# Performance work log

Hardware: AMD Instinct MI355X
Metric: run time of the kernel (lower is better)

Reference implementation:

```python
import jax, jax.numpy as jnp
import numpy as np

B, L, D, H, A = 4, 2048, 1024, 16, 64  # batch, seq, d_model, n_head, d_head


def setup_inputs() -> dict:
    key = jax.random.key(0)
    ks = jax.random.split(key, 6)
    scale = 1.0 / np.sqrt(D)
    return {
        "xq": jax.random.normal(ks[0], (B, L, D), dtype=jnp.float32),
        "xkv": jax.random.normal(ks[1], (B, L, D), dtype=jnp.float32),
        "Q": jax.random.normal(ks[2], (D, H, A), dtype=jnp.float32) * scale,
        "K": jax.random.normal(ks[3], (D, H, A), dtype=jnp.float32) * scale,
        "V": jax.random.normal(ks[4], (D, H, A), dtype=jnp.float32) * scale,
        "O": jax.random.normal(ks[5], (D, H, A), dtype=jnp.float32) * scale,
    }


def reference(xq, xkv, Q, K, V, O):
    # embed: 'dha, ...ld -> ...lha'
    q = jnp.einsum('dha,bld->blha', Q, xq)
    k = jnp.einsum('dha,bld->blha', K, xkv)
    v = jnp.einsum('dha,bld->blha', V, xkv)
    # outer: '...lha, ...mha -> ...hlm'  (full LxL score matrix, no scaling in source)
    scores = jnp.einsum('blha,bmha->bhlm', q, k)
    attn = jax.nn.softmax(scores, axis=-1)  # dropout p=0 (eval)
    # score: '...hlm, ...mha -> ...lha'
    ctx = jnp.einsum('bhlm,bmha->blha', attn, v)
    # output: '...dha, ...lha -> ...ld'
    return jnp.einsum('dha,blha->bld', O, ctx)
```

## Files before the change

### kernel.cpp

```cpp
#include <hip/hip_runtime.h>
#include <math.h>

typedef __bf16 bf16;
typedef bf16 bf16x8 __attribute__((ext_vector_type(8)));
typedef bf16 bf16x4 __attribute__((ext_vector_type(4)));
typedef float f32x4 __attribute__((ext_vector_type(4)));
typedef float f32x16 __attribute__((ext_vector_type(16)));

#define B_ 4
#define L_ 2048
#define D_ 1024
#define H_ 16
#define A_ 64
#define HA_ 1024
#define BL_ 8192
#define LOG2E 1.44269504088896340736f

__device__ __forceinline__ void gload16(const void* g, void* l) {
  __builtin_amdgcn_global_load_lds((const __attribute__((address_space(1))) void*)g,
                                   (__attribute__((address_space(3))) void*)l,
                                   16, 0, 0);
}

__device__ __forceinline__ unsigned cvt_pk_bf16(float lo, float hi) {
  unsigned r;
  asm volatile("v_cvt_pk_bf16_f32 %0, %1, %2" : "=v"(r) : "v"(lo), "v"(hi));
  return r;
}

__device__ __forceinline__ void permswap(unsigned& a, unsigned& b) {
  asm volatile("v_permlane32_swap_b32 %0, %1" : "+v"(a), "+v"(b));
}

__global__ __launch_bounds__(256) void cast_all(const float* __restrict__ xq,
                                                const float* __restrict__ xkv,
                                                const float* __restrict__ ow,
                                                bf16* __restrict__ xq_b,
                                                bf16* __restrict__ xkv_b,
                                                bf16* __restrict__ wo_b) {
  const int NX = BL_ * D_ / 8;
  const int NW = D_ * HA_ / 8;
  int i = blockIdx.x * blockDim.x + threadIdx.x;
  const float* src;
  bf16* dst;
  int j;
  if (i < NX) { src = xq; dst = xq_b; j = i; }
  else if (i < 2 * NX) { src = xkv; dst = xkv_b; j = i - NX; }
  else if (i < 2 * NX + NW) { src = ow; dst = wo_b; j = i - 2 * NX; }
  else return;
  const float4* s = reinterpret_cast<const float4*>(src) + (size_t)j * 2;
  float4 a = s[0], b = s[1];
  bf16x8 o;
  o[0] = (bf16)a.x; o[1] = (bf16)a.y; o[2] = (bf16)a.z; o[3] = (bf16)a.w;
  o[4] = (bf16)b.x; o[5] = (bf16)b.y; o[6] = (bf16)b.z; o[7] = (bf16)b.w;
  *reinterpret_cast<bf16x8*>(dst + (size_t)j * 8) = o;
}

__global__ __launch_bounds__(256) void transpose_cast_w3(const float* __restrict__ wq,
                                                         const float* __restrict__ wk,
                                                         const float* __restrict__ wv,
                                                         bf16* __restrict__ oq,
                                                         bf16* __restrict__ ok,
                                                         bf16* __restrict__ ov) {
  __shared__ float tile[32][33];
  const int z = blockIdx.z;
  const float* w = (z == 0) ? wq : (z == 1) ? wk : wv;
  bf16* wt = (z == 0) ? oq : (z == 1) ? ok : ov;
  const float scale = (z == 0) ? LOG2E : 1.0f;
  const int d0 = blockIdx.y * 32, h0 = blockIdx.x * 32;
  const int tx = threadIdx.x, ty = threadIdx.y;
  #pragma unroll
  for (int j = 0; j < 4; j++)
    tile[ty + j * 8][tx] = w[(size_t)(d0 + ty + j * 8) * HA_ + h0 + tx];
  __syncthreads();
  #pragma unroll
  for (int j = 0; j < 4; j++)
    wt[(size_t)(h0 + ty + j * 8) * D_ + d0 + tx] = (bf16)(tile[tx][ty + j * 8] * scale);
}

template <int MODE>
__device__ __forceinline__ void gemm_bt_core(const bf16* __restrict__ Ap,
                                             const bf16* __restrict__ Bp,
                                             void* __restrict__ Cp,
                                             int m0, int n0) {
  const int K = 1024;
  __shared__ __align__(16) bf16 As[128 * 32];
  __shared__ __align__(16) bf16 Bs[128 * 32];
  const int tid = threadIdx.x;
  const int lane = tid & 63, w = tid >> 6;
  const int wr = w >> 1, wc = w & 1;
  const int g = lane >> 4, c = lane & 15;
  f32x4 acc[4][4] = {};
  const int srow = tid >> 2, sch = tid & 3;
  const int sw0 = (sch ^ (srow & 3)) * 8;
  for (int k0 = 0; k0 < K; k0 += 32) {
    gload16(Ap + (size_t)(m0 + srow) * K + k0 + sw0, As + tid * 8);
    gload16(Ap + (size_t)(m0 + 64 + srow) * K + k0 + sw0, As + (256 + tid) * 8);
    gload16(Bp + (size_t)(n0 + srow) * K + k0 + sw0, Bs + tid * 8);
    gload16(Bp + (size_t)(n0 + 64 + srow) * K + k0 + sw0, Bs + (256 + tid) * 8);
    __syncthreads();
    bf16x8 af[4], bfr[4];
    #pragma unroll
    for (int m = 0; m < 4; m++)
      af[m] = *reinterpret_cast<const bf16x8*>(As + (wr * 64 + m * 16 + c) * 32 + ((g ^ (c & 3)) * 8));
    #pragma unroll
    for (int n = 0; n < 4; n++)
      bfr[n] = *reinterpret_cast<const bf16x8*>(Bs + (wc * 64 + n * 16 + c) * 32 + ((g ^ (c & 3)) * 8));
    #pragma unroll
    for (int m = 0; m < 4; m++)
      #pragma unroll
      for (int n = 0; n < 4; n++)
        acc[m][n] = __builtin_amdgcn_mfma_f32_16x16x32_bf16(af[m], bfr[n], acc[m][n], 0, 0, 0);
    __syncthreads();
  }
  #pragma unroll
  for (int m = 0; m < 4; m++) {
    #pragma unroll
    for (int n = 0; n < 4; n++) {
      if (MODE == 2) {
        int row0 = m0 + wr * 64 + m * 16 + g * 4;
        int col = n0 + wc * 64 + n * 16 + c;
        int b = row0 >> 11, l0 = row0 & 2047, h = col >> 6, a = col & 63;
        bf16x4 o4;
        #pragma unroll
        for (int i = 0; i < 4; i++) o4[i] = (bf16)acc[m][n][i];
        *reinterpret_cast<bf16x4*>((bf16*)Cp + ((size_t)(b * H_ + h) * A_ + a) * L_ + l0) = o4;
      } else {
        #pragma unroll
        for (int i = 0; i < 4; i++) {
          int row = m0 + wr * 64 + m * 16 + g * 4 + i;
          int col = n0 + wc * 64 + n * 16 + c;
          float v = acc[m][n][i];
          if (MODE == 0) {
            int b = row >> 11, l = row & 2047, h = col >> 6, a = col & 63;
            ((bf16*)Cp)[(((size_t)b * H_ + h) * L_ + l) * A_ + a] = (bf16)v;
          } else {
            ((float*)Cp)[(size_t)row * 1024 + col] = v;
          }
        }
      }
    }
  }
}

__device__ __forceinline__ void xcd_mn(int id, int& m0, int& n0) {
  int xcd = id & 7, j = id >> 3;
  m0 = (xcd * 8 + (j >> 3)) * 128;
  n0 = (j & 7) * 128;
}

__global__ __launch_bounds__(256, 2) void gemm_proj(const bf16* xq_b, const bf16* xkv_b,
                                                    const bf16* wq, const bf16* wk, const bf16* wv,
                                                    bf16* qb, bf16* kb, bf16* vtb) {
  int m0, n0;
  xcd_mn(blockIdx.x, m0, n0);
  const int z = blockIdx.z;
  if (z == 0)      gemm_bt_core<0>(xq_b, wq, qb, m0, n0);
  else if (z == 1) gemm_bt_core<0>(xkv_b, wk, kb, m0, n0);
  else             gemm_bt_core<2>(xkv_b, wv, vtb, m0, n0);
}

__global__ __launch_bounds__(256, 2) void gemm_out_k(const bf16* ctx, const bf16* wo, float* out) {
  int m0, n0;
  xcd_mn(blockIdx.x, m0, n0);
  gemm_bt_core<1>(ctx, wo, out, m0, n0);
}

__device__ __forceinline__ void pa_build(const f32x16& s, bf16x8& f0, bf16x8& f1) {
  #pragma unroll
  for (int sl = 0; sl < 2; sl++) {
    unsigned a0 = cvt_pk_bf16(s[8 * sl + 0], s[8 * sl + 1]);
    unsigned b0 = cvt_pk_bf16(s[8 * sl + 4], s[8 * sl + 5]);
    permswap(a0, b0);
    unsigned a1 = cvt_pk_bf16(s[8 * sl + 2], s[8 * sl + 3]);
    unsigned b1 = cvt_pk_bf16(s[8 * sl + 6], s[8 * sl + 7]);
    permswap(a1, b1);
    uint4 v; v.x = a0; v.y = a1; v.z = b0; v.w = b1;
    if (sl == 0) f0 = __builtin_bit_cast(bf16x8, v);
    else         f1 = __builtin_bit_cast(bf16x8, v);
  }
}

__global__ __launch_bounds__(512, 2) void attn_kernel(const bf16* __restrict__ qg,
                                                      const bf16* __restrict__ kg,
                                                      const bf16* __restrict__ vtg,
                                                      bf16* __restrict__ ctx) {
  __shared__ __align__(16) bf16 Ks[2][64 * 64];
  __shared__ __align__(16) bf16 Vs[2][64 * 64];
  const int tid = threadIdx.x;
  const int lane = tid & 63;
  const int w = tid >> 6;
  const int c = lane & 31;
  const int hi = lane >> 5;
  const int cs7 = c & 7;
  const int bh = blockIdx.x;
  const int q0 = blockIdx.y * 256;
  const bf16* qh = qg + (size_t)bh * L_ * A_;
  const bf16* kh = kg + (size_t)bh * L_ * A_;
  const bf16* vh = vtg + (size_t)bh * A_ * L_;

  const int qrow = q0 + w * 32 + c;
  bf16x8 qf[4];
  #pragma unroll
  for (int ds = 0; ds < 4; ds++)
    qf[ds] = *reinterpret_cast<const bf16x8*>(qh + (size_t)qrow * A_ + ds * 16 + hi * 8);

  bf16x8 ones;
  #pragma unroll
  for (int j = 0; j < 8; j++) ones[j] = (bf16)1.0f;

  f32x16 oacc0 = {}, oacc1 = {};
  f32x16 ssum = {};

  int koA[4], koB[4];
  #pragma unroll
  for (int ds = 0; ds < 4; ds++) {
    koA[ds] = c * 64 + ((2 * ds + hi) ^ cs7) * 8;
    koB[ds] = (32 + c) * 64 + ((2 * ds + hi) ^ cs7) * 8;
  }

  const int sr = tid >> 3, sc = tid & 7;
  const int ss = (sc ^ (sr & 7)) * 8;
  const bf16* ksrc = kh + (size_t)sr * A_ + ss;
  const bf16* vsrc = vh + (size_t)sr * L_ + ss;

  gload16(ksrc, &Ks[0][tid * 8]);
  gload16(vsrc, &Vs[0][tid * 8]);
  __syncthreads();
  int cur = 0;

  for (int t = 0; t < L_ / 64; t++) {
    if (t < L_ / 64 - 1) {
      gload16(ksrc + (size_t)(t + 1) * 4096, &Ks[cur ^ 1][tid * 8]);
      gload16(vsrc + (size_t)(t + 1) * 64, &Vs[cur ^ 1][tid * 8]);
    }
    const bf16* Kc = Ks[cur];
    const bf16* Vc = Vs[cur];

    f32x16 s0 = {}, s1 = {};
    __builtin_amdgcn_s_setprio(1);
    #pragma unroll
    for (int ds = 0; ds < 4; ds++) {
      bf16x8 k0 = *reinterpret_cast<const bf16x8*>(Kc + koA[ds]);
      bf16x8 k1 = *reinterpret_cast<const bf16x8*>(Kc + koB[ds]);
      s0 = __builtin_amdgcn_mfma_f32_32x32x16_bf16(k0, qf[ds], s0, 0, 0, 0);
      s1 = __builtin_amdgcn_mfma_f32_32x32x16_bf16(k1, qf[ds], s1, 0, 0, 0);
    }
    __builtin_amdgcn_s_setprio(0);

    #pragma unroll
    for (int r = 0; r < 16; r++) {
      s0[r] = __builtin_amdgcn_exp2f(s0[r]);
      s1[r] = __builtin_amdgcn_exp2f(s1[r]);
    }

    bf16x8 paf0, paf1, paf2, paf3;
    pa_build(s0, paf0, paf1);
    pa_build(s1, paf2, paf3);

    __builtin_amdgcn_s_setprio(1);
    #pragma unroll
    for (int ks = 0; ks < 4; ks++) {
      const bf16x8 pa = (ks == 0) ? paf0 : (ks == 1) ? paf1 : (ks == 2) ? paf2 : paf3;
      bf16x8 v0 = *reinterpret_cast<const bf16x8*>(Vc + koA[ks]);
      bf16x8 v1 = *reinterpret_cast<const bf16x8*>(Vc + koB[ks]);
      oacc0 = __builtin_amdgcn_mfma_f32_32x32x16_bf16(v0, pa, oacc0, 0, 0, 0);
      oacc1 = __builtin_amdgcn_mfma_f32_32x32x16_bf16(v1, pa, oacc1, 0, 0, 0);
      ssum = __builtin_amdgcn_mfma_f32_32x32x16_bf16(ones, pa, ssum, 0, 0, 0);
    }
    __builtin_amdgcn_s_setprio(0);

    __syncthreads();
    cur ^= 1;
  }

  float inv = 1.f / ssum[0];
  const int b = bh >> 4, h = bh & 15;
  bf16* crow = ctx + (((size_t)b * L_ + qrow) * H_ + h) * A_;
  #pragma unroll
  for (int n = 0; n < 2; n++) {
    #pragma unroll
    for (int rq = 0; rq < 4; rq++) {
      bf16x4 o4;
      #pragma unroll
      for (int j = 0; j < 4; j++) {
        float v = (n == 0) ? oacc0[rq * 4 + j] : oacc1[rq * 4 + j];
        o4[j] = (bf16)(v * inv);
      }
      *reinterpret_cast<bf16x4*>(crow + n * 32 + rq * 8 + hi * 4) = o4;
    }
  }
}

extern "C" void kernel_launch(void* const* d_in, const int* in_sizes, int n_in,
                              void* d_out, int out_size, void* d_ws, size_t ws_size,
                              hipStream_t stream) {
  const float* xq = (const float*)d_in[0];
  const float* xkv = (const float*)d_in[1];
  const float* Qw = (const float*)d_in[2];
  const float* Kw = (const float*)d_in[3];
  const float* Vw = (const float*)d_in[4];
  const float* Ow = (const float*)d_in[5];
  float* out = (float*)d_out;

  char* ws = (char*)d_ws;
  const size_t SZ16 = (size_t)BL_ * HA_ * sizeof(bf16);
  const size_t SZW = (size_t)D_ * HA_ * sizeof(bf16);
  bf16* xq_b = (bf16*)(ws);
  bf16* xkv_b = (bf16*)(ws + SZ16);
  bf16* wq_t = (bf16*)(ws + 2 * SZ16);
  bf16* wk_t = (bf16*)(ws + 2 * SZ16 + SZW);
  bf16* wv_t = (bf16*)(ws + 2 * SZ16 + 2 * SZW);
  bf16* wo_b = (bf16*)(ws + 2 * SZ16 + 3 * SZW);
  bf16* qb = (bf16*)(ws + 2 * SZ16 + 4 * SZW);
  bf16* kb = qb + (size_t)BL_ * HA_;
  bf16* vtb = kb + (size_t)BL_ * HA_;
  bf16* ctxb = xkv_b;

  const int NCAST = (2 * BL_ * D_ + D_ * HA_) / 8;
  cast_all<<<(NCAST + 255) / 256, 256, 0, stream>>>(xq, xkv, Ow, xq_b, xkv_b, wo_b);
  transpose_cast_w3<<<dim3(32, 32, 3), dim3(32, 8), 0, stream>>>(Qw, Kw, Vw, wq_t, wk_t, wv_t);

  gemm_proj<<<dim3(512, 1, 3), 256, 0, stream>>>(xq_b, xkv_b, wq_t, wk_t, wv_t, qb, kb, vtb);
  attn_kernel<<<dim3(64, 8), 512, 0, stream>>>(qb, kb, vtb, ctxb);
  gemm_out_k<<<512, 256, 0, stream>>>(ctxb, wo_b, out);
}
```

Measured before the change: 194.9 us.

## Merge cast and weight-transpose kernels; fuse K and V projections sharing A tile

```diff
diff --git a/kernel.cpp b/kernel.cpp
--- a/kernel.cpp
+++ b/kernel.cpp
@@ -15,6 +15,7 @@
 #define HA_ 1024
 #define BL_ 8192
 #define LOG2E 1.44269504088896340736f
+#define NCASTB 8704
 
 __device__ __forceinline__ void gload16(const void* g, void* l) {
   __builtin_amdgcn_global_load_lds((const __attribute__((address_space(1))) void*)g,
@@ -32,50 +33,54 @@
   asm volatile("v_permlane32_swap_b32 %0, %1" : "+v"(a), "+v"(b));
 }
 
-__global__ __launch_bounds__(256) void cast_all(const float* __restrict__ xq,
+__global__ __launch_bounds__(256) void prep_all(const float* __restrict__ xq,
                                                 const float* __restrict__ xkv,
                                                 const float* __restrict__ ow,
+                                                const float* __restrict__ wq,
+                                                const float* __restrict__ wk,
+                                                const float* __restrict__ wv,
                                                 bf16* __restrict__ xq_b,
                                                 bf16* __restrict__ xkv_b,
-                                                bf16* __restrict__ wo_b) {
+                                                bf16* __restrict__ wo_b,
+                                                bf16* __restrict__ oq,
+                                                bf16* __restrict__ ok,
+                                                bf16* __restrict__ ov) {
+  __shared__ float tile[32][33];
   const int NX = BL_ * D_ / 8;
   const int NW = D_ * HA_ / 8;
-  int i = blockIdx.x * blockDim.x + threadIdx.x;
-  const float* src;
-  bf16* dst;
-  int j;
-  if (i < NX) { src = xq; dst = xq_b; j = i; }
-  else if (i < 2 * NX) { src = xkv; dst = xkv_b; j = i - NX; }
-  else if (i < 2 * NX + NW) { src = ow; dst = wo_b; j = i - 2 * NX; }
-  else return;
-  const float4* s = reinterpret_cast<const float4*>(src) + (size_t)j * 2;
-  float4 a = s[0], b = s[1];
-  bf16x8 o;
-  o[0] = (bf16)a.x; o[1] = (bf16)a.y; o[2] = (bf16)a.z; o[3] = (bf16)a.w;
-  o[4] = (bf16)b.x; o[5] = (bf16)b.y; o[6] = (bf16)b.z; o[7] = (bf16)b.w;
-  *reinterpret_cast<bf16x8*>(dst + (size_t)j * 8) = o;
-}
-
-__global__ __launch_bounds__(256) void transpose_cast_w3(const float* __restrict__ wq,
-                                                         const float* __restrict__ wk,
-                                                         const float* __restrict__ wv,
-                                                         bf16* __restrict__ oq,
-                                                         bf16* __restrict__ ok,
-                                                         bf16* __restrict__ ov) {
-  __shared__ float tile[32][33];
-  const int z = blockIdx.z;
-  const float* w = (z == 0) ? wq : (z == 1) ? wk : wv;
-  bf16* wt = (z == 0) ? oq : (z == 1) ? ok : ov;
-  const float scale = (z == 0) ? LOG2E : 1.0f;
-  const int d0 = blockIdx.y * 32, h0 = blockIdx.x * 32;
-  const int tx = threadIdx.x, ty = threadIdx.y;
-  #pragma unroll
-  for (int j = 0; j < 4; j++)
-    tile[ty + j * 8][tx] = w[(size_t)(d0 + ty + j * 8) * HA_ + h0 + tx];
-  __syncthreads();
-  #pragma unroll
-  for (int j = 0; j < 4; j++)
-    wt[(size_t)(h0 + ty + j * 8) * D_ + d0 + tx] = (bf16)(tile[tx][ty + j * 8] * scale);
+  int bid = blockIdx.x;
+  if (bid < NCASTB) {
+    int i = bid * 256 + threadIdx.x;
+    const float* src;
+    bf16* dst;
+    int j;
+    if (i < NX) { src = xq; dst = xq_b; j = i; }
+    else if (i < 2 * NX) { src = xkv; dst = xkv_b; j = i - NX; }
+    else if (i < 2 * NX + NW) { src = ow; dst = wo_b; j = i - 2 * NX; }
+    else return;
+    const float4* s = reinterpret_cast<const float4*>(src) + (size_t)j * 2;
+    float4 a = s[0], b = s[1];
+    bf16x8 o;
+    o[0] = (bf16)a.x; o[1] = (bf16)a.y; o[2] = (bf16)a.z; o[3] = (bf16)a.w;
+    o[4] = (bf16)b.x; o[5] = (bf16)b.y; o[6] = (bf16)b.z; o[7] = (bf16)b.w;
+    *reinterpret_cast<bf16x8*>(dst + (size_t)j * 8) = o;
+  } else {
+    int t3 = bid - NCASTB;
+    int z = t3 >> 10;
+    int rem = t3 & 1023;
+    const float* w = (z == 0) ? wq : (z == 1) ? wk : wv;
+    bf16* wt = (z == 0) ? oq : (z == 1) ? ok : ov;
+    const float scale = (z == 0) ? LOG2E : 1.0f;
+    const int h0 = (rem & 31) * 32, d0 = (rem >> 5) * 32;
+    const int tx = threadIdx.x & 31, ty = threadIdx.x >> 5;
+    #pragma unroll
+    for (int j = 0; j < 4; j++)
+      tile[ty + j * 8][tx] = w[(size_t)(d0 + ty + j * 8) * HA_ + h0 + tx];
+    __syncthreads();
+    #pragma unroll
+    for (int j = 0; j < 4; j++)
+      wt[(size_t)(h0 + ty + j * 8) * D_ + d0 + tx] = (bf16)(tile[tx][ty + j * 8] * scale);
+  }
 }
 
 template <int MODE>
@@ -117,28 +122,82 @@
   for (int m = 0; m < 4; m++) {
     #pragma unroll
     for (int n = 0; n < 4; n++) {
-      if (MODE == 2) {
-        int row0 = m0 + wr * 64 + m * 16 + g * 4;
+      #pragma unroll
+      for (int i = 0; i < 4; i++) {
+        int row = m0 + wr * 64 + m * 16 + g * 4 + i;
         int col = n0 + wc * 64 + n * 16 + c;
-        int b = row0 >> 11, l0 = row0 & 2047, h = col >> 6, a = col & 63;
-        bf16x4 o4;
-        #pragma unroll
-        for (int i = 0; i < 4; i++) o4[i] = (bf16)acc[m][n][i];
-        *reinterpret_cast<bf16x4*>((bf16*)Cp + ((size_t)(b * H_ + h) * A_ + a) * L_ + l0) = o4;
-      } else {
-        #pragma unroll
-        for (int i = 0; i < 4; i++) {
-          int row = m0 + wr * 64 + m * 16 + g * 4 + i;
-          int col = n0 + wc * 64 + n * 16 + c;
-          float v = acc[m][n][i];
-          if (MODE == 0) {
-            int b = row >> 11, l = row & 2047, h = col >> 6, a = col & 63;
-            ((bf16*)Cp)[(((size_t)b * H_ + h) * L_ + l) * A_ + a] = (bf16)v;
-          } else {
-            ((float*)Cp)[(size_t)row * 1024 + col] = v;
-          }
+        float v = acc[m][n][i];
+        if (MODE == 0) {
+          int b = row >> 11, l = row & 2047, h = col >> 6, a = col & 63;
+          ((bf16*)Cp)[(((size_t)b * H_ + h) * L_ + l) * A_ + a] = (bf16)v;
+        } else {
+          ((float*)Cp)[(size_t)row * 1024 + col] = v;
         }
       }
+    }
+  }
+}
+
+__device__ __forceinline__ void gemm_kv_fused(const bf16* __restrict__ Ap,
+                                              const bf16* __restrict__ Bkp,
+                                              const bf16* __restrict__ Bvp,
+                                              bf16* __restrict__ kb,
+                                              bf16* __restrict__ vtb,
+                                              int m0, int n0) {
+  const int K = 1024;
+  __shared__ __align__(16) bf16 As2[128 * 32];
+  __shared__ __align__(16) bf16 Bks[128 * 32];
+  __shared__ __align__(16) bf16 Bvs[128 * 32];
+  const int tid = threadIdx.x;
+  const int lane = tid & 63, w = tid >> 6;
+  const int wr = w >> 1, wc = w & 1;
+  const int g = lane >> 4, c = lane & 15;
+  f32x4 acck[4][4] = {}, accv[4][4] = {};
+  const int srow = tid >> 2, sch = tid & 3;
+  const int sw0 = (sch ^ (srow & 3)) * 8;
+  for (int k0 = 0; k0 < K; k0 += 32) {
+    gload16(Ap + (size_t)(m0 + srow) * K + k0 + sw0, As2 + tid * 8);
+    gload16(Ap + (size_t)(m0 + 64 + srow) * K + k0 + sw0, As2 + (256 + tid) * 8);
+    gload16(Bkp + (size_t)(n0 + srow) * K + k0 + sw0, Bks + tid * 8);
+    gload16(Bkp + (size_t)(n0 + 64 + srow) * K + k0 + sw0, Bks + (256 + tid) * 8);
+    gload16(Bvp + (size_t)(n0 + srow) * K + k0 + sw0, Bvs + tid * 8);
+    gload16(Bvp + (size_t)(n0 + 64 + srow) * K + k0 + sw0, Bvs + (256 + tid) * 8);
+    __syncthreads();
+    bf16x8 af[4], bkf[4], bvf[4];
+    #pragma unroll
+    for (int m = 0; m < 4; m++)
+      af[m] = *reinterpret_cast<const bf16x8*>(As2 + (wr * 64 + m * 16 + c) * 32 + ((g ^ (c & 3)) * 8));
+    #pragma unroll
+    for (int n = 0; n < 4; n++) {
+      bkf[n] = *reinterpret_cast<const bf16x8*>(Bks + (wc * 64 + n * 16 + c) * 32 + ((g ^ (c & 3)) * 8));
+      bvf[n] = *reinterpret_cast<const bf16x8*>(Bvs + (wc * 64 + n * 16 + c) * 32 + ((g ^ (c & 3)) * 8));
+    }
+    #pragma unroll
+    for (int m = 0; m < 4; m++)
+      #pragma unroll
+      for (int n = 0; n < 4; n++) {
+        acck[m][n] = __builtin_amdgcn_mfma_f32_16x16x32_bf16(af[m], bkf[n], acck[m][n], 0, 0, 0);
+        accv[m][n] = __builtin_amdgcn_mfma_f32_16x16x32_bf16(af[m], bvf[n], accv[m][n], 0, 0, 0);
+      }
+    __syncthreads();
+  }
+  #pragma unroll
+  for (int m = 0; m < 4; m++) {
+    #pragma unroll
+    for (int n = 0; n < 4; n++) {
+      int row0 = m0 + wr * 64 + m * 16 + g * 4;
+      int col = n0 + wc * 64 + n * 16 + c;
+      int b = row0 >> 11, h = col >> 6, a = col & 63;
+      #pragma unroll
+      for (int i = 0; i < 4; i++) {
+        int l = (row0 + i) & 2047;
+        kb[(((size_t)b * H_ + h) * L_ + l) * A_ + a] = (bf16)acck[m][n][i];
+      }
+      int l0 = row0 & 2047;
+      bf16x4 o4;
+      #pragma unroll
+      for (int i = 0; i < 4; i++) o4[i] = (bf16)accv[m][n][i];
+      *reinterpret_cast<bf16x4*>(vtb + ((size_t)(b * H_ + h) * A_ + a) * L_ + l0) = o4;
     }
   }
 }
@@ -154,10 +213,8 @@
                                                     bf16* qb, bf16* kb, bf16* vtb) {
   int m0, n0;
   xcd_mn(blockIdx.x, m0, n0);
-  const int z = blockIdx.z;
-  if (z == 0)      gemm_bt_core<0>(xq_b, wq, qb, m0, n0);
-  else if (z == 1) gemm_bt_core<0>(xkv_b, wk, kb, m0, n0);
-  else             gemm_bt_core<2>(xkv_b, wv, vtb, m0, n0);
+  if (blockIdx.z == 0) gemm_bt_core<0>(xq_b, wq, qb, m0, n0);
+  else                 gemm_kv_fused(xkv_b, wk, wv, kb, vtb, m0, n0);
 }
 
 __global__ __launch_bounds__(256, 2) void gemm_out_k(const bf16* ctx, const bf16* wo, float* out) {
@@ -317,11 +374,9 @@
   bf16* vtb = kb + (size_t)BL_ * HA_;
   bf16* ctxb = xkv_b;
 
-  const int NCAST = (2 * BL_ * D_ + D_ * HA_) / 8;
-  cast_all<<<(NCAST + 255) / 256, 256, 0, stream>>>(xq, xkv, Ow, xq_b, xkv_b, wo_b);
-  transpose_cast_w3<<<dim3(32, 32, 3), dim3(32, 8), 0, stream>>>(Qw, Kw, Vw, wq_t, wk_t, wv_t);
-
-  gemm_proj<<<dim3(512, 1, 3), 256, 0, stream>>>(xq_b, xkv_b, wq_t, wk_t, wv_t, qb, kb, vtb);
+  prep_all<<<NCASTB + 3072, 256, 0, stream>>>(xq, xkv, Ow, Qw, Kw, Vw,
+                                              xq_b, xkv_b, wo_b, wq_t, wk_t, wv_t);
+  gemm_proj<<<dim3(512, 1, 2), 256, 0, stream>>>(xq_b, xkv_b, wq_t, wk_t, wv_t, qb, kb, vtb);
   attn_kernel<<<dim3(64, 8), 512, 0, stream>>>(qb, kb, vtb, ctxb);
   gemm_out_k<<<512, 256, 0, stream>>>(ctxb, wo_b, out);
 }
```

After: 191.4 us. No clear change (-1.8%).
